# Kernel tuning notes

Measured on AMD Instinct MI355X. Metric: run time of the kernel, lower is better.

## Reference

```python
import jax, jax.numpy as jnp
import numpy as np

N_NODES = 10000
N_EDGES = 160000
MUL = 128            # multiplicity of 0e and 1o node feature irreps
N_RADIAL = 8
AVG_NEIGH = 16.0
INV_SQRT3 = float(1.0 / np.sqrt(3.0))  # w3j(1,1,0) contraction factor (component norm)


def setup_inputs() -> dict:
    key = jax.random.key(0)
    ks = jax.random.split(key, 16)
    node_feats = jax.random.normal(ks[0], (N_NODES, MUL + 3 * MUL), jnp.float32)
    edge_attrs = jax.random.normal(ks[1], (N_EDGES, 4), jnp.float32)      # sph harms l=0,1
    edge_feats = jax.random.normal(ks[2], (N_EDGES, N_RADIAL), jnp.float32)
    lengths = jax.random.uniform(ks[3], (N_EDGES, 1), jnp.float32)
    edge_index = jax.random.randint(ks[4], (2, N_EDGES), 0, N_NODES)
    d_in = 2 * MUL + N_RADIAL + 1  # 265: sender scalars + receiver scalars + radial + length
    def lin(k, sh):
        return jax.random.normal(k, sh, jnp.float32) / np.sqrt(sh[0])
    # last MLP layer: variance_scaling(scale=1e-6, fan_avg, uniform)
    fan_avg = (MUL + 4 * MUL) / 2.0
    lim = float(np.sqrt(3.0 * (0.001 ** 2) / fan_avg))
    return dict(
        node_feats=node_feats, edge_attrs=edge_attrs, edge_feats=edge_feats,
        lengths=lengths, edge_index=edge_index,
        W_scalar=lin(ks[5], (MUL, MUL)),
        W_up0=lin(ks[6], (MUL, MUL)),
        W_up1=lin(ks[7], (MUL, MUL)),
        W_mlp1=lin(ks[8], (d_in, MUL)), b_mlp1=jnp.zeros((MUL,), jnp.float32),
        W_mlp2=lin(ks[9], (MUL, MUL)), b_mlp2=jnp.zeros((MUL,), jnp.float32),
        W_mlp3=jax.random.uniform(ks[10], (MUL, 4 * MUL), jnp.float32, -lim, lim),
        W_out0=lin(ks[11], (2 * MUL, MUL)),
        W_out1=lin(ks[12], (2 * MUL, MUL)),
    )


def reference(node_feats, edge_attrs, edge_feats, lengths, edge_index,
              W_scalar, W_up0, W_up1, W_mlp1, b_mlp1, W_mlp2, b_mlp2, W_mlp3,
              W_out0, W_out1):
    sender, receiver = edge_index[0], edge_index[1]
    s_in = node_feats[:, :MUL]                        # [N, 128] 0e
    v_in = node_feats[:, MUL:].reshape(-1, MUL, 3)    # [N, 128, 3] 1o
    inv = 1.0 / np.sqrt(MUL)
    # linear_scalar / linear_up (e3nn Linear, element path normalization)
    node_scalars = (s_in @ W_scalar) * inv            # [N, 128]
    s_up = (s_in @ W_up0) * inv                       # [N, 128]
    v_up = jnp.einsum('nui,uw->nwi', v_in, W_up1) * inv  # [N, 128, 3]
    # per-edge MLP -> tensor-product weights (Dense-SiLU-Dense-SiLU-Dense)
    mlp_in = jnp.concatenate([node_scalars[sender], node_scalars[receiver],
                              edge_feats, lengths], axis=-1)  # [E, 265]
    h = jax.nn.silu(mlp_in @ W_mlp1 + b_mlp1)
    h = jax.nn.silu(h @ W_mlp2 + b_mlp2)
    tpw = h @ W_mlp3                                  # [E, 512]
    w0, w1, w2, w3 = jnp.split(tpw, 4, axis=-1)       # one [E,128] block per TP path
    # gather sender features; split edge sph harms
    se = s_up[sender]                                 # [E, 128]
    ve = v_up[sender]                                 # [E, 128, 3]
    y0 = edge_attrs[:, 0:1]                           # [E, 1]
    y1 = edge_attrs[:, 1:4]                           # [E, 3]
    # equivariant 'uvu' tensor product (component irrep normalization)
    m0a = w0 * se * y0                                                # 0e x 0e -> 0e
    m0b = w3 * jnp.einsum('eui,ei->eu', ve, y1) * INV_SQRT3           # 1o x 1o -> 0e
    m1a = (w1 * se)[:, :, None] * y1[:, None, :]                      # 0e x 1o -> 1o
    m1b = (w2 * y0)[:, :, None] * ve                                  # 1o x 0e -> 1o
    mji = jnp.concatenate([m0a, m0b,
                           m1a.reshape(N_EDGES, -1),
                           m1b.reshape(N_EDGES, -1)], axis=-1)        # [E, 1024]
    # scatter-sum aggregate over receivers
    msg = jax.ops.segment_sum(mji, receiver, num_segments=N_NODES)    # [N, 1024]
    ms = msg[:, :2 * MUL]                             # [N, 256]  (two 0e blocks)
    mv = msg[:, 2 * MUL:].reshape(-1, 2 * MUL, 3)     # [N, 256, 3] (two 1o blocks)
    # final e3nn Linear (irreps_mid -> target) then / avg_num_neighbors
    inv2 = 1.0 / np.sqrt(2 * MUL)
    out_s = (ms @ W_out0) * (inv2 / AVG_NEIGH)                        # [N, 128]
    out_v = jnp.einsum('nui,uw->nwi', mv, W_out1) * (inv2 / AVG_NEIGH)  # [N, 128, 3]
    # reshape_irreps: [N, mul, (lmax+1)^2] = [N, 128, 4]
    return jnp.concatenate([out_s[:, :, None], out_v], axis=-1)
```

## Files before the change

### kernel.cpp

```cpp
#include <hip/hip_runtime.h>

#define N_NODESC 10000
#define N_EDGESC 160000
#define NBLK_TOT 2500
#define NP       (N_NODESC*128)
#define INV128   0.08838834764831845f
#define INV_SQRT3C 0.5773502691896258f
#define SCALE_OUT 0.00390625f

typedef __attribute__((ext_vector_type(8))) short bf16x8;
typedef __attribute__((ext_vector_type(4))) float f32x4;

__device__ __forceinline__ float silu_f(float x) {
  return x / (1.f + __expf(-x));
}
__device__ __forceinline__ ushort f2bf_rne(float x) {
  uint u = __float_as_uint(x);
  uint r = (u + 0x7FFFu + ((u >> 16) & 1u)) >> 16;
  return (ushort)r;
}
__device__ __forceinline__ float bf2f(ushort h) {
  return __uint_as_float(((uint)h) << 16);
}

__global__ __launch_bounds__(256) void k_hist(const int* __restrict__ eidx,
                                              int* __restrict__ deg) {
  int e = blockIdx.x * 256 + threadIdx.x;
  if (e < N_EDGESC) atomicAdd(&deg[eidx[N_EDGESC + e]], 1);
}

__global__ __launch_bounds__(1024) void k_scan(const int* __restrict__ deg,
                                               int* __restrict__ row_start,
                                               int* __restrict__ cursor) {
  __shared__ int buf[1024];
  const int t = threadIdx.x;
  for (int i = t; i < N_NODESC; i += 1024) cursor[i] = 0;
  int d[10];
  int loc = 0;
  #pragma unroll
  for (int i = 0; i < 10; i++) {
    int n = t * 10 + i;
    d[i] = (n < N_NODESC) ? deg[n] : 0;
    loc += d[i];
  }
  buf[t] = loc;
  __syncthreads();
  int v = loc;
  for (int off = 1; off < 1024; off <<= 1) {
    int u = (t >= off) ? buf[t - off] : 0;
    __syncthreads();
    v += u;
    buf[t] = v;
    __syncthreads();
  }
  int run = v - loc;
  #pragma unroll
  for (int i = 0; i < 10; i++) {
    int n = t * 10 + i;
    if (n < N_NODESC) row_start[n] = run;
    run += d[i];
  }
  if (t == 1023) row_start[N_NODESC] = v;
}

__global__ __launch_bounds__(256) void k_scatter(const int* __restrict__ eidx,
                                                 const int* __restrict__ row_start,
                                                 int* __restrict__ cursor,
                                                 int* __restrict__ perm) {
  int e = blockIdx.x * 256 + threadIdx.x;
  if (e < N_EDGESC) {
    int r = eidx[N_EDGESC + e];
    int pos = row_start[r] + atomicAdd(&cursor[r], 1);
    perm[pos] = e;
  }
}

__global__ __launch_bounds__(256) void k_sortseg(int* __restrict__ perm,
                                                 const int* __restrict__ row_start) {
  int n = blockIdx.x * 256 + threadIdx.x;
  if (n >= N_NODESC) return;
  int s = row_start[n], e = row_start[n + 1];
  for (int i = s + 1; i < e; i++) {
    int key = perm[i];
    int j = i - 1;
    while (j >= s && perm[j] > key) { perm[j + 1] = perm[j]; j--; }
    perm[j + 1] = key;
  }
}

__global__ __launch_bounds__(256) void k_wcomp(
    const float* __restrict__ Wsc, const float* __restrict__ W1,
    ushort* __restrict__ TT) {
  __shared__ float sA2[64][132];
  __shared__ float sW2[128][128];
  const int rh = blockIdx.x;
  const int wb = blockIdx.y;
  for (int idx = threadIdx.x; idx < 128 * 32; idx += 256) {
    int k = idx >> 5, fc = (idx & 31) << 2;
    *(float4*)&sW2[k][fc] = *(const float4*)&W1[(wb * 128 + k) * 128 + fc];
  }
  for (int idx = threadIdx.x; idx < 64 * 32; idx += 256) {
    int i = idx >> 5, fc = (idx & 31) << 2;
    *(float4*)&sA2[i][fc] = *(const float4*)&Wsc[(rh * 64 + i) * 128 + fc];
  }
  __syncthreads();
  const int r0 = (threadIdx.x >> 4) * 4;
  const int c0 = (threadIdx.x & 15) * 8;
  float acc[4][8] = {};
  #pragma unroll 4
  for (int k = 0; k < 128; k++) {
    float a[4];
    #pragma unroll
    for (int j = 0; j < 4; j++) a[j] = sA2[r0 + j][k];
    float w[8];
    *(float4*)&w[0] = *(const float4*)&sW2[k][c0];
    *(float4*)&w[4] = *(const float4*)&sW2[k][c0 + 4];
    #pragma unroll
    for (int j = 0; j < 4; j++)
      #pragma unroll
      for (int c = 0; c < 8; c++) acc[j][c] += a[j] * w[c];
  }
  #pragma unroll
  for (int j = 0; j < 4; j++) {
    int u = rh * 64 + r0 + j;
    #pragma unroll
    for (int c = 0; c < 8; c++) {
      float v = acc[j][c];
      ushort hi = f2bf_rne(v);
      TT[(wb * 2 + 0) * 16384 + (c0 + c) * 128 + u] = hi;
      TT[(wb * 2 + 1) * 16384 + (c0 + c) * 128 + u] = f2bf_rne(v - bf2f(hi));
    }
  }
}

__global__ __launch_bounds__(256) void k_wprep(
    const float* __restrict__ W2, const float* __restrict__ W3,
    const float* __restrict__ Wu0, const float* __restrict__ Wu1,
    const float* __restrict__ Wo0, const float* __restrict__ Wo1,
    ushort* __restrict__ TT) {
  int id = blockIdx.x * 256 + threadIdx.x;
  if (id < 16384) {
    int k = id >> 7, n = id & 127;
    float v = W2[k * 128 + n];
    ushort hi = f2bf_rne(v);
    TT[4 * 16384 + n * 128 + k] = hi;
    TT[5 * 16384 + n * 128 + k] = f2bf_rne(v - bf2f(hi));
  } else if (id < 81920) {
    int s = id - 16384;
    int k = s >> 9, col = s & 511;
    int cb = col >> 7, n = col & 127;
    TT[(6 + cb) * 16384 + n * 128 + k] = f2bf_rne(W3[k * 512 + col]);
  } else if (id < 114688) {
    int t = id - 81920;
    int w = t >> 14, r = t & 16383;
    int k = r >> 7, n = r & 127;
    const float* W = w ? Wu1 : Wu0;
    float v = W[k * 128 + n];
    ushort hi = f2bf_rne(v);
    TT[(10 + w * 2) * 16384 + n * 128 + k] = hi;
    TT[(11 + w * 2) * 16384 + n * 128 + k] = f2bf_rne(v - bf2f(hi));
  } else if (id < 180224) {
    int t = id - 114688;
    int w = t >> 15, r = t & 32767;
    int k = r >> 7, n = r & 127;
    const float* W = w ? Wo1 : Wo0;
    float v = W[k * 128 + n];
    int kh = k >> 7, kk = k & 127;
    ushort hi = f2bf_rne(v);
    TT[(16 + w * 4 + kh * 2) * 16384 + n * 128 + kk] = hi;
    TT[(17 + w * 4 + kh * 2) * 16384 + n * 128 + kk] = f2bf_rne(v - bf2f(hi));
  }
}

#define GEMM_PASS1(ACC)                                                        \
  _Pragma("unroll") for (int s = 0; s < 4; s++) {                              \
    bf16x8 ah = *(const bf16x8*)&sAh[ar][s * 32 + lq * 8];                     \
    _Pragma("unroll") for (int nt = 0; nt < 8; nt++) {                         \
      bf16x8 bb = *(const bf16x8*)&sB[nt * 16 + ln][s * 32 + lq * 8];          \
      ACC[nt] = __builtin_amdgcn_mfma_f32_16x16x32_bf16(ah, bb, ACC[nt], 0, 0, 0); \
    }                                                                          \
  }

#define STAGEB(T) { uint4 tv[8];                                               \
  _Pragma("unroll") for (int i = 0; i < 8; i++)                                \
    tv[i] = ttp[(T) * 2048 + cid + 256 * i];                                   \
  _Pragma("unroll") for (int i = 0; i < 8; i++) {                              \
    int c = cid + 256 * i;                                                     \
    *(uint4*)&sB[c >> 4][(c & 15) * 8] = tv[i]; } }

__global__ __launch_bounds__(256, 3) void k_node_up(
    const float* __restrict__ nf,
    const ushort* __restrict__ TT,
    float* __restrict__ P1s,
    float* __restrict__ P1r,
    float* __restrict__ SU,
    float* __restrict__ VU)
{
  __shared__ ushort sAh[64][132];
  __shared__ ushort sB[128][132];
  const int n0 = blockIdx.x * 64;
  const int which = blockIdx.y;
  const int cid = threadIdx.x;
  const int wid = cid >> 6;
  const int lane = cid & 63;
  const int lq = lane >> 4;
  const int ln = lane & 15;
  const int ar = wid * 16 + ln;
  const uint4* ttp = (const uint4*)TT;

  if (which == 0) {
    for (int idx = cid; idx < 64 * 32; idx += 256) {
      int r = idx >> 5, fc = (idx & 31) << 2;
      int n = n0 + r;
      float4 v = {0.f, 0.f, 0.f, 0.f};
      if (n < N_NODESC) v = *(const float4*)&nf[(size_t)n * 512 + fc];
      float vv[4] = {v.x, v.y, v.z, v.w};
      #pragma unroll
      for (int j = 0; j < 4; j++) sAh[r][fc + j] = f2bf_rne(vv[j]);
    }
    for (int g = 0; g < 3; g++) {
      if (g) __syncthreads();
      const int tA = (g == 2) ? 10 : g * 2;
      STAGEB(tA)
      __syncthreads();
      f32x4 acc[8];
      #pragma unroll
      for (int nt = 0; nt < 8; nt++) acc[nt] = (f32x4){0.f, 0.f, 0.f, 0.f};
      GEMM_PASS1(acc)
      __syncthreads();
      STAGEB(tA + 1)
      __syncthreads();
      GEMM_PASS1(acc)
      float* op = (g == 0) ? P1s : ((g == 1) ? P1r : SU);
      #pragma unroll
      for (int q = 0; q < 4; q++) {
        int n = n0 + wid * 16 + lq * 4 + q;
        if (n < N_NODESC) {
          #pragma unroll
          for (int nt = 0; nt < 8; nt++)
            op[(size_t)n * 128 + nt * 16 + ln] = acc[nt][q] * INV128;
        }
      }
    }
  } else {
    int comp = which - 1;
    for (int idx = cid; idx < 64 * 128; idx += 256) {
      int r = idx >> 7, u = idx & 127;
      int n = n0 + r;
      float v = (n < N_NODESC) ? nf[(size_t)n * 512 + 128 + u * 3 + comp] : 0.f;
      sAh[r][u] = f2bf_rne(v);
    }
    STAGEB(12)
    __syncthreads();
    f32x4 acc[8];
    #pragma unroll
    for (int nt = 0; nt < 8; nt++) acc[nt] = (f32x4){0.f, 0.f, 0.f, 0.f};
    GEMM_PASS1(acc)
    __syncthreads();
    STAGEB(13)
    __syncthreads();
    GEMM_PASS1(acc)
    float* op = VU + (size_t)comp * NP;
    #pragma unroll
    for (int q = 0; q < 4; q++) {
      int n = n0 + wid * 16 + lq * 4 + q;
      if (n < N_NODESC) {
        #pragma unroll
        for (int nt = 0; nt < 8; nt++)
          op[(size_t)n * 128 + nt * 16 + ln] = acc[nt][q] * INV128;
      }
    }
  }
}

#define REDUCE(P, MI) {                                                        \
  const int ntask = sNseg << 7;                                                \
  for (int task = cid; task < ntask; task += 256) {                            \
    const int si = task >> 7, col = task & 127;                                \
    const int s = sSegStart[si], e = sSegStart[si + 1];                        \
    float sum = 0.f;                                                           \
    int e2 = s;                                                                \
    for (; e2 + 8 <= e; e2 += 8) {                                             \
      float m0 = sMsg[e2][col],     m1 = sMsg[e2 + 1][col];                    \
      float m2 = sMsg[e2 + 2][col], m3 = sMsg[e2 + 3][col];                    \
      float m4 = sMsg[e2 + 4][col], m5 = sMsg[e2 + 5][col];                    \
      float m6 = sMsg[e2 + 6][col], m7 = sMsg[e2 + 7][col];                    \
      if ((MI) >= 0) {                                                         \
        const int mi = (MI) >= 0 ? (MI) : 0;                                   \
        sum += m0 * sY4[e2][mi];     sum += m1 * sY4[e2 + 1][mi];              \
        sum += m2 * sY4[e2 + 2][mi]; sum += m3 * sY4[e2 + 3][mi];              \
        sum += m4 * sY4[e2 + 4][mi]; sum += m5 * sY4[e2 + 5][mi];              \
        sum += m6 * sY4[e2 + 6][mi]; sum += m7 * sY4[e2 + 7][mi];              \
      } else { sum += m0; sum += m1; sum += m2; sum += m3;                     \
               sum += m4; sum += m5; sum += m6; sum += m7; }                   \
    }                                                                          \
    for (; e2 < e; e2++) {                                                     \
      float mv = sMsg[e2][col];                                                \
      sum += ((MI) >= 0) ? mv * sY4[e2][(MI) >= 0 ? (MI) : 0] : mv;            \
    }                                                                          \
    if (si == 0 && contF)                                                      \
      CONT[(size_t)gblk * 1024 + (P) * 128 + col] = sum;                       \
    else                                                                       \
      MSG[(size_t)(P) * NP + (size_t)sSegNode[si] * 128 + col] = sum;          \
  } }

#define REDUCE3 {                                                              \
  const int ntask = sNseg << 7;                                                \
  for (int task = cid; task < ntask; task += 256) {                            \
    const int si = task >> 7, col = task & 127;                                \
    const int s = sSegStart[si], e = sSegStart[si + 1];                        \
    float s0 = 0.f, s1 = 0.f, s2 = 0.f;                                        \
    int e2 = s;                                                                \
    for (; e2 + 4 <= e; e2 += 4) {                                             \
      _Pragma("unroll") for (int u = 0; u < 4; u++) {                          \
        float mv = sMsg[e2 + u][col];                                          \
        s0 += mv * sY4[e2 + u][1];                                             \
        s1 += mv * sY4[e2 + u][2];                                             \
        s2 += mv * sY4[e2 + u][3];                                             \
      }                                                                        \
    }                                                                          \
    for (; e2 < e; e2++) {                                                     \
      float mv = sMsg[e2][col];                                                \
      s0 += mv * sY4[e2][1]; s1 += mv * sY4[e2][2]; s2 += mv * sY4[e2][3];     \
    }                                                                          \
    if (si == 0 && contF) {                                                    \
      CONT[(size_t)gblk * 1024 + 2 * 128 + col] = s0;                          \
      CONT[(size_t)gblk * 1024 + 3 * 128 + col] = s1;                          \
      CONT[(size_t)gblk * 1024 + 4 * 128 + col] = s2;                          \
    } else {                                                                   \
      size_t nb = (size_t)sSegNode[si] * 128 + col;                            \
      MSG[2 * (size_t)NP + nb] = s0;                                           \
      MSG[3 * (size_t)NP + nb] = s1;                                           \
      MSG[4 * (size_t)NP + nb] = s2;                                           \
    }                                                                          \
  } }

__global__ __launch_bounds__(256, 3) void k_edge_fused(
    const float* __restrict__ P1s,
    const float* __restrict__ P1r,
    const float* __restrict__ SU,
    const float* __restrict__ VU,
    const float* __restrict__ ef,
    const float* __restrict__ len,
    const float* __restrict__ ea,
    const int* __restrict__ eidx,
    const int* __restrict__ perm,
    const int* __restrict__ row_start,
    const float* __restrict__ W1,
    const float* __restrict__ b1,
    const float* __restrict__ b2,
    const ushort* __restrict__ TT,
    float* __restrict__ MSG,
    float* __restrict__ CONT)
{
  __shared__ ushort sAh[64][132];
  __shared__ ushort sB[128][132];
  __shared__ float sY4[64][4];
  __shared__ int sSnd[64], sRcv[64], sEid[64];
  __shared__ int sSegStart[65], sSegNode[64];
  __shared__ int sNseg, sContFirst;
  float (*sMsg)[132] = (float (*)[132])&sB[0][0];

  const int bid = blockIdx.x;
  const int xcd = bid & 7, sub = bid >> 3;
  const int gblk = (xcd < 4) ? (xcd * 313 + sub)
                             : (1252 + (xcd - 4) * 312 + sub);
  const int j0 = gblk * 64;
  const int cid = threadIdx.x;
  const int wid = cid >> 6;
  const int lane = cid & 63;
  const int lq = lane >> 4;
  const int ln = lane & 15;
  const int ar = wid * 16 + ln;
  const uint4* ttp = (const uint4*)TT;

  if (cid < 64) {
    int r = cid;
    int e = perm[j0 + r];
    int snd = eidx[e];
    int rcv = eidx[N_EDGESC + e];
    sSnd[r] = snd;
    sRcv[r] = rcv;
    sEid[r] = e;
    *(float4*)&sY4[r][0] = *(const float4*)&ea[(size_t)e * 4];
    int prev = __shfl_up(rcv, 1);
    bool flag = (r == 0) || (rcv != prev);
    unsigned long long mask = __ballot(flag ? 1 : 0);
    if (flag) {
      int rank = __popcll(mask & ((1ull << r) - 1ull));
      sSegStart[rank] = r;
      sSegNode[rank] = rcv;
    }
    if (r == 0) {
      sNseg = __popcll(mask);
      sContFirst = (row_start[rcv] != j0) ? 1 : 0;
    }
    if (r == 63) sSegStart[__popcll(mask)] = 64;
  }
  __syncthreads();
  const bool contF = (sContFirst != 0);

  for (int idx = cid; idx < 64 * 32; idx += 256) {
    int r = idx >> 5, c4 = (idx & 31) << 2;
    int ns = sSnd[r], nr = sRcv[r];
    float4 a = *(const float4*)&P1s[(size_t)ns * 128 + c4];
    float4 b = *(const float4*)&P1r[(size_t)nr * 128 + c4];
    int e = sEid[r];
    float el[9];
    float4 e0 = *(const float4*)&ef[(size_t)e * 8];
    float4 e1 = *(const float4*)&ef[(size_t)e * 8 + 4];
    el[0] = e0.x; el[1] = e0.y; el[2] = e0.z; el[3] = e0.w;
    el[4] = e1.x; el[5] = e1.y; el[6] = e1.z; el[7] = e1.w;
    el[8] = len[e];
    float4 bb = *(const float4*)&b1[c4];
    float v[4] = {a.x + b.x + bb.x, a.y + b.y + bb.y,
                  a.z + b.z + bb.z, a.w + b.w + bb.w};
    #pragma unroll
    for (int t = 0; t < 9; t++) {
      float4 wt = *(const float4*)&W1[(size_t)(256 + t) * 128 + c4];
      float elt = el[t];
      v[0] += elt * wt.x; v[1] += elt * wt.y;
      v[2] += elt * wt.z; v[3] += elt * wt.w;
    }
    #pragma unroll
    for (int j = 0; j < 4; j++)
      sAh[r][c4 + j] = f2bf_rne(silu_f(v[j]));
  }
  STAGEB(4)
  __syncthreads();

  f32x4 acc2[8];
  #pragma unroll
  for (int nt = 0; nt < 8; nt++) acc2[nt] = (f32x4){0.f, 0.f, 0.f, 0.f};
  GEMM_PASS1(acc2)
  __syncthreads();
  STAGEB(5)
  __syncthreads();
  GEMM_PASS1(acc2)
  __syncthreads();
  #pragma unroll
  for (int nt = 0; nt < 8; nt++) {
    int col = nt * 16 + ln;
    float bb2 = b2[col];
    #pragma unroll
    for (int q = 0; q < 4; q++) {
      int rr = wid * 16 + lq * 4 + q;
      sAh[rr][col] = f2bf_rne(silu_f(acc2[nt][q] + bb2));
    }
  }

  int erow[4], esnd[4];
  float y0r[4], y1r3[4][3];
  #pragma unroll
  for (int q = 0; q < 4; q++) {
    int rr = wid * 16 + lq * 4 + q;
    erow[q] = rr;
    esnd[q] = sSnd[rr];
    y0r[q] = sY4[rr][0];
    #pragma unroll
    for (int i = 0; i < 3; i++) y1r3[q][i] = sY4[rr][1 + i];
  }
  float se[4][8];
  #pragma unroll
  for (int q = 0; q < 4; q++)
    #pragma unroll
    for (int nt = 0; nt < 8; nt++)
      se[q][nt] = SU[(size_t)esnd[q] * 128 + nt * 16 + ln];
  float dacc[4][8];

  STAGEB(6)
  __syncthreads();

  {
    f32x4 acc3[8];
    #pragma unroll
    for (int nt = 0; nt < 8; nt++) acc3[nt] = (f32x4){0.f, 0.f, 0.f, 0.f};
    GEMM_PASS1(acc3)
    __syncthreads();
    #pragma unroll
    for (int q = 0; q < 4; q++)
      #pragma unroll
      for (int nt = 0; nt < 8; nt++)
        sMsg[erow[q]][nt * 16 + ln] = acc3[nt][q] * se[q][nt] * y0r[q];
    __syncthreads();
    REDUCE(0, -1)
    __syncthreads();
    STAGEB(7)
    __syncthreads();
  }
  {
    f32x4 acc3[8];
    #pragma unroll
    for (int nt = 0; nt < 8; nt++) acc3[nt] = (f32x4){0.f, 0.f, 0.f, 0.f};
    GEMM_PASS1(acc3)
    __syncthreads();
    #pragma unroll
    for (int q = 0; q < 4; q++)
      #pragma unroll
      for (int nt = 0; nt < 8; nt++)
        sMsg[erow[q]][nt * 16 + ln] = acc3[nt][q] * se[q][nt];
    __syncthreads();
    REDUCE3
    __syncthreads();
    STAGEB(8)
    __syncthreads();
  }
  {
    f32x4 acc3[8];
    #pragma unroll
    for (int nt = 0; nt < 8; nt++) acc3[nt] = (f32x4){0.f, 0.f, 0.f, 0.f};
    GEMM_PASS1(acc3)
    __syncthreads();
    for (int pi = 0; pi < 3; pi++) {
      float vu[4][8];
      #pragma unroll
      for (int q = 0; q < 4; q++)
        #pragma unroll
        for (int nt = 0; nt < 8; nt++) {
          vu[q][nt] = VU[(size_t)pi * NP + (size_t)esnd[q] * 128 + nt * 16 + ln];
          if (pi == 0) dacc[q][nt] = vu[q][nt] * y1r3[q][0];
          else dacc[q][nt] += vu[q][nt] * y1r3[q][pi];
        }
      #pragma unroll
      for (int q = 0; q < 4; q++)
        #pragma unroll
        for (int nt = 0; nt < 8; nt++)
          sMsg[erow[q]][nt * 16 + ln] = acc3[nt][q] * vu[q][nt];
      __syncthreads();
      if (pi == 0) { REDUCE(5, 0) }
      else if (pi == 1) { REDUCE(6, 0) }
      else { REDUCE(7, 0) }
      __syncthreads();
    }
    STAGEB(9)
    __syncthreads();
  }
  {
    f32x4 acc3[8];
    #pragma unroll
    for (int nt = 0; nt < 8; nt++) acc3[nt] = (f32x4){0.f, 0.f, 0.f, 0.f};
    GEMM_PASS1(acc3)
    __syncthreads();
    #pragma unroll
    for (int q = 0; q < 4; q++)
      #pragma unroll
      for (int nt = 0; nt < 8; nt++)
        sMsg[erow[q]][nt * 16 + ln] = acc3[nt][q] * dacc[q][nt] * INV_SQRT3C;
    __syncthreads();
    REDUCE(1, -1)
  }
}

__global__ __launch_bounds__(256) void k_fixup(float* __restrict__ MSG,
                                               const float* __restrict__ CONT,
                                               const int* __restrict__ row_start) {
  int t = blockIdx.x * 256 + threadIdx.x;
  int n = t >> 5;
  int c4 = (t & 31) * 4;
  if (n >= N_NODESC) return;
  int s = row_start[n], e = row_start[n + 1];
  if (e <= s) return;
  int b0 = s >> 6, b1 = (e - 1) >> 6;
  if (b1 <= b0) return;
  for (int p = 0; p < 8; p++) {
    float4 v = *(float4*)&MSG[(size_t)p * NP + (size_t)n * 128 + c4];
    for (int b = b0 + 1; b <= b1; b++) {
      const float4 u = *(const float4*)&CONT[(size_t)b * 1024 + p * 128 + c4];
      v.x += u.x; v.y += u.y; v.z += u.z; v.w += u.w;
    }
    *(float4*)&MSG[(size_t)p * NP + (size_t)n * 128 + c4] = v;
  }
}

__global__ __launch_bounds__(256, 3) void k_out(
    const float* __restrict__ MSG,
    const ushort* __restrict__ TT,
    float* __restrict__ out)
{
  __shared__ ushort sAh[64][132];
  __shared__ ushort sB[128][132];
  const int n0 = blockIdx.x * 64;
  const int y = blockIdx.y;
  const int cid = threadIdx.x;
  const int wid = cid >> 6;
  const int lane = cid & 63;
  const int lq = lane >> 4;
  const int ln = lane & 15;
  const int ar = wid * 16 + ln;
  const uint4* ttp = (const uint4*)TT;
  const int pA = (y == 0) ? 0 : (1 + y);
  const int pB = (y == 0) ? 1 : (4 + y);
  const int tbase = 16 + ((y == 0) ? 0 : 4);

  f32x4 acc[8];
  #pragma unroll
  for (int nt = 0; nt < 8; nt++) acc[nt] = (f32x4){0.f, 0.f, 0.f, 0.f};

  for (int kh = 0; kh < 2; kh++) {
    if (kh) __syncthreads();
    const int p = kh ? pB : pA;
    for (int idx = cid; idx < 64 * 32; idx += 256) {
      int r = idx >> 5, fc = (idx & 31) << 2;
      int n = n0 + r;
      float4 v = {0.f, 0.f, 0.f, 0.f};
      if (n < N_NODESC) v = *(const float4*)&MSG[(size_t)p * NP + (size_t)n * 128 + fc];
      float vv[4] = {v.x, v.y, v.z, v.w};
      #pragma unroll
      for (int j = 0; j < 4; j++) sAh[r][fc + j] = f2bf_rne(vv[j]);
    }
    STAGEB(tbase + kh * 2)
    __syncthreads();
    GEMM_PASS1(acc)
    __syncthreads();
    STAGEB(tbase + kh * 2 + 1)
    __syncthreads();
    GEMM_PASS1(acc)
  }
  #pragma unroll
  for (int q = 0; q < 4; q++) {
    int n = n0 + wid * 16 + lq * 4 + q;
    if (n < N_NODESC) {
      #pragma unroll
      for (int nt = 0; nt < 8; nt++)
        out[(size_t)n * 512 + (size_t)(nt * 16 + ln) * 4 + y] = acc[nt][q] * SCALE_OUT;
    }
  }
}

extern "C" void kernel_launch(void* const* d_in, const int* in_sizes, int n_in,
                              void* d_out, int out_size, void* d_ws, size_t ws_size,
                              hipStream_t stream) {
  const float* nf  = (const float*)d_in[0];
  const float* ea  = (const float*)d_in[1];
  const float* ef  = (const float*)d_in[2];
  const float* len = (const float*)d_in[3];
  const int*   ei  = (const int*)d_in[4];
  const float* Wsc = (const float*)d_in[5];
  const float* Wu0 = (const float*)d_in[6];
  const float* Wu1 = (const float*)d_in[7];
  const float* W1  = (const float*)d_in[8];
  const float* b1  = (const float*)d_in[9];
  const float* W2  = (const float*)d_in[10];
  const float* b2  = (const float*)d_in[11];
  const float* W3  = (const float*)d_in[12];
  const float* Wo0 = (const float*)d_in[13];
  const float* Wo1 = (const float*)d_in[14];
  float* out = (float*)d_out;
  float* ws  = (float*)d_ws;

  const size_t NPs = (size_t)NP;
  float* P1s  = ws;
  float* P1r  = ws + NPs;
  float* SU   = ws + 2 * NPs;
  float* VU   = ws + 3 * NPs;
  float* MSG  = ws + 6 * NPs;
  float* CONT = ws + 14 * NPs;
  ushort* TT  = (ushort*)(CONT + (size_t)NBLK_TOT * 1024);
  int* perm      = (int*)(TT + 24 * 16384);
  int* deg       = perm + N_EDGESC;
  int* cursor    = deg + N_NODESC;
  int* row_start = cursor + N_NODESC;

  hipMemsetAsync(deg, 0, N_NODESC * sizeof(int), stream);
  hipMemsetAsync(MSG, 0, 8 * NPs * sizeof(float), stream);

  k_hist<<<(N_EDGESC + 255) / 256, 256, 0, stream>>>(ei, deg);
  k_scan<<<1, 1024, 0, stream>>>(deg, row_start, cursor);
  k_scatter<<<(N_EDGESC + 255) / 256, 256, 0, stream>>>(ei, row_start, cursor, perm);
  k_sortseg<<<(N_NODESC + 255) / 256, 256, 0, stream>>>(perm, row_start);
  k_wcomp<<<dim3(2, 2), 256, 0, stream>>>(Wsc, W1, TT);
  k_wprep<<<704, 256, 0, stream>>>(W2, W3, Wu0, Wu1, Wo0, Wo1, TT);

  k_node_up<<<dim3(157, 4), 256, 0, stream>>>(nf, TT, P1s, P1r, SU, VU);

  k_edge_fused<<<NBLK_TOT, 256, 0, stream>>>(P1s, P1r, SU, VU, ef, len, ea, ei,
                                             perm, row_start, W1, b1, b2, TT,
                                             MSG, CONT);

  k_fixup<<<(N_NODESC * 32 + 255) / 256, 256, 0, stream>>>(MSG, CONT, row_start);
  k_out<<<dim3(157, 4), 256, 0, stream>>>(MSG, TT, out);
}
```

Measured before the change: 312.6 us.

## Merge small preprocessing kernels and drop the message-buffer memset

Folds the degree histogram into the weight-prep kernel, and the per-segment insertion sort into k_node_up as an extra grid slice, which cuts two kernel launches. The 8*NP-float memset of MSG is removed; k_fixup now writes zeros for nodes with no incoming edges. This relies on k_edge_fused writing every MSG row that has edges, and the sort running inside node_up is correct only because that kernel does not read perm.

```diff
diff --git a/kernel.cpp b/kernel.cpp
--- a/kernel.cpp
+++ b/kernel.cpp
@@ -23,122 +23,19 @@
   return __uint_as_float(((uint)h) << 16);
 }
 
-__global__ __launch_bounds__(256) void k_hist(const int* __restrict__ eidx,
-                                              int* __restrict__ deg) {
-  int e = blockIdx.x * 256 + threadIdx.x;
-  if (e < N_EDGESC) atomicAdd(&deg[eidx[N_EDGESC + e]], 1);
-}
-
-__global__ __launch_bounds__(1024) void k_scan(const int* __restrict__ deg,
-                                               int* __restrict__ row_start,
-                                               int* __restrict__ cursor) {
-  __shared__ int buf[1024];
-  const int t = threadIdx.x;
-  for (int i = t; i < N_NODESC; i += 1024) cursor[i] = 0;
-  int d[10];
-  int loc = 0;
-  #pragma unroll
-  for (int i = 0; i < 10; i++) {
-    int n = t * 10 + i;
-    d[i] = (n < N_NODESC) ? deg[n] : 0;
-    loc += d[i];
-  }
-  buf[t] = loc;
-  __syncthreads();
-  int v = loc;
-  for (int off = 1; off < 1024; off <<= 1) {
-    int u = (t >= off) ? buf[t - off] : 0;
-    __syncthreads();
-    v += u;
-    buf[t] = v;
-    __syncthreads();
-  }
-  int run = v - loc;
-  #pragma unroll
-  for (int i = 0; i < 10; i++) {
-    int n = t * 10 + i;
-    if (n < N_NODESC) row_start[n] = run;
-    run += d[i];
-  }
-  if (t == 1023) row_start[N_NODESC] = v;
-}
-
-__global__ __launch_bounds__(256) void k_scatter(const int* __restrict__ eidx,
-                                                 const int* __restrict__ row_start,
-                                                 int* __restrict__ cursor,
-                                                 int* __restrict__ perm) {
-  int e = blockIdx.x * 256 + threadIdx.x;
-  if (e < N_EDGESC) {
-    int r = eidx[N_EDGESC + e];
-    int pos = row_start[r] + atomicAdd(&cursor[r], 1);
-    perm[pos] = e;
-  }
-}
-
-__global__ __launch_bounds__(256) void k_sortseg(int* __restrict__ perm,
-                                                 const int* __restrict__ row_start) {
-  int n = blockIdx.x * 256 + threadIdx.x;
-  if (n >= N_NODESC) return;
-  int s = row_start[n], e = row_start[n + 1];
-  for (int i = s + 1; i < e; i++) {
-    int key = perm[i];
-    int j = i - 1;
-    while (j >= s && perm[j] > key) { perm[j + 1] = perm[j]; j--; }
-    perm[j + 1] = key;
-  }
-}
-
-__global__ __launch_bounds__(256) void k_wcomp(
-    const float* __restrict__ Wsc, const float* __restrict__ W1,
-    ushort* __restrict__ TT) {
-  __shared__ float sA2[64][132];
-  __shared__ float sW2[128][128];
-  const int rh = blockIdx.x;
-  const int wb = blockIdx.y;
-  for (int idx = threadIdx.x; idx < 128 * 32; idx += 256) {
-    int k = idx >> 5, fc = (idx & 31) << 2;
-    *(float4*)&sW2[k][fc] = *(const float4*)&W1[(wb * 128 + k) * 128 + fc];
-  }
-  for (int idx = threadIdx.x; idx < 64 * 32; idx += 256) {
-    int i = idx >> 5, fc = (idx & 31) << 2;
-    *(float4*)&sA2[i][fc] = *(const float4*)&Wsc[(rh * 64 + i) * 128 + fc];
-  }
-  __syncthreads();
-  const int r0 = (threadIdx.x >> 4) * 4;
-  const int c0 = (threadIdx.x & 15) * 8;
-  float acc[4][8] = {};
-  #pragma unroll 4
-  for (int k = 0; k < 128; k++) {
-    float a[4];
-    #pragma unroll
-    for (int j = 0; j < 4; j++) a[j] = sA2[r0 + j][k];
-    float w[8];
-    *(float4*)&w[0] = *(const float4*)&sW2[k][c0];
-    *(float4*)&w[4] = *(const float4*)&sW2[k][c0 + 4];
-    #pragma unroll
-    for (int j = 0; j < 4; j++)
-      #pragma unroll
-      for (int c = 0; c < 8; c++) acc[j][c] += a[j] * w[c];
-  }
-  #pragma unroll
-  for (int j = 0; j < 4; j++) {
-    int u = rh * 64 + r0 + j;
-    #pragma unroll
-    for (int c = 0; c < 8; c++) {
-      float v = acc[j][c];
-      ushort hi = f2bf_rne(v);
-      TT[(wb * 2 + 0) * 16384 + (c0 + c) * 128 + u] = hi;
-      TT[(wb * 2 + 1) * 16384 + (c0 + c) * 128 + u] = f2bf_rne(v - bf2f(hi));
-    }
-  }
-}
-
-__global__ __launch_bounds__(256) void k_wprep(
+__global__ __launch_bounds__(256) void k_histprep(
+    const int* __restrict__ eidx, int* __restrict__ deg,
     const float* __restrict__ W2, const float* __restrict__ W3,
     const float* __restrict__ Wu0, const float* __restrict__ Wu1,
     const float* __restrict__ Wo0, const float* __restrict__ Wo1,
     ushort* __restrict__ TT) {
-  int id = blockIdx.x * 256 + threadIdx.x;
+  const int bid = blockIdx.x;
+  if (bid < 625) {
+    int e = bid * 256 + threadIdx.x;
+    if (e < N_EDGESC) atomicAdd(&deg[eidx[N_EDGESC + e]], 1);
+    return;
+  }
+  int id = (bid - 625) * 256 + threadIdx.x;
   if (id < 16384) {
     int k = id >> 7, n = id & 127;
     float v = W2[k * 128 + n];
@@ -172,6 +69,97 @@
   }
 }
 
+__global__ __launch_bounds__(1024) void k_scan(const int* __restrict__ deg,
+                                               int* __restrict__ row_start,
+                                               int* __restrict__ cursor) {
+  __shared__ int buf[1024];
+  const int t = threadIdx.x;
+  for (int i = t; i < N_NODESC; i += 1024) cursor[i] = 0;
+  int d[10];
+  int loc = 0;
+  #pragma unroll
+  for (int i = 0; i < 10; i++) {
+    int n = t * 10 + i;
+    d[i] = (n < N_NODESC) ? deg[n] : 0;
+    loc += d[i];
+  }
+  buf[t] = loc;
+  __syncthreads();
+  int v = loc;
+  for (int off = 1; off < 1024; off <<= 1) {
+    int u = (t >= off) ? buf[t - off] : 0;
+    __syncthreads();
+    v += u;
+    buf[t] = v;
+    __syncthreads();
+  }
+  int run = v - loc;
+  #pragma unroll
+  for (int i = 0; i < 10; i++) {
+    int n = t * 10 + i;
+    if (n < N_NODESC) row_start[n] = run;
+    run += d[i];
+  }
+  if (t == 1023) row_start[N_NODESC] = v;
+}
+
+__global__ __launch_bounds__(256) void k_scatter(const int* __restrict__ eidx,
+                                                 const int* __restrict__ row_start,
+                                                 int* __restrict__ cursor,
+                                                 int* __restrict__ perm) {
+  int e = blockIdx.x * 256 + threadIdx.x;
+  if (e < N_EDGESC) {
+    int r = eidx[N_EDGESC + e];
+    int pos = row_start[r] + atomicAdd(&cursor[r], 1);
+    perm[pos] = e;
+  }
+}
+
+__global__ __launch_bounds__(256) void k_wcomp(
+    const float* __restrict__ Wsc, const float* __restrict__ W1,
+    ushort* __restrict__ TT) {
+  __shared__ float sA2[64][132];
+  __shared__ float sW2[128][128];
+  const int rh = blockIdx.x;
+  const int wb = blockIdx.y;
+  for (int idx = threadIdx.x; idx < 128 * 32; idx += 256) {
+    int k = idx >> 5, fc = (idx & 31) << 2;
+    *(float4*)&sW2[k][fc] = *(const float4*)&W1[(wb * 128 + k) * 128 + fc];
+  }
+  for (int idx = threadIdx.x; idx < 64 * 32; idx += 256) {
+    int i = idx >> 5, fc = (idx & 31) << 2;
+    *(float4*)&sA2[i][fc] = *(const float4*)&Wsc[(rh * 64 + i) * 128 + fc];
+  }
+  __syncthreads();
+  const int r0 = (threadIdx.x >> 4) * 4;
+  const int c0 = (threadIdx.x & 15) * 8;
+  float acc[4][8] = {};
+  #pragma unroll 4
+  for (int k = 0; k < 128; k++) {
+    float a[4];
+    #pragma unroll
+    for (int j = 0; j < 4; j++) a[j] = sA2[r0 + j][k];
+    float w[8];
+    *(float4*)&w[0] = *(const float4*)&sW2[k][c0];
+    *(float4*)&w[4] = *(const float4*)&sW2[k][c0 + 4];
+    #pragma unroll
+    for (int j = 0; j < 4; j++)
+      #pragma unroll
+      for (int c = 0; c < 8; c++) acc[j][c] += a[j] * w[c];
+  }
+  #pragma unroll
+  for (int j = 0; j < 4; j++) {
+    int u = rh * 64 + r0 + j;
+    #pragma unroll
+    for (int c = 0; c < 8; c++) {
+      float v = acc[j][c];
+      ushort hi = f2bf_rne(v);
+      TT[(wb * 2 + 0) * 16384 + (c0 + c) * 128 + u] = hi;
+      TT[(wb * 2 + 1) * 16384 + (c0 + c) * 128 + u] = f2bf_rne(v - bf2f(hi));
+    }
+  }
+}
+
 #define GEMM_PASS1(ACC)                                                        \
   _Pragma("unroll") for (int s = 0; s < 4; s++) {                              \
     bf16x8 ah = *(const bf16x8*)&sAh[ar][s * 32 + lq * 8];                     \
@@ -194,7 +182,9 @@
     float* __restrict__ P1s,
     float* __restrict__ P1r,
     float* __restrict__ SU,
-    float* __restrict__ VU)
+    float* __restrict__ VU,
+    int* __restrict__ perm,
+    const int* __restrict__ row_start)
 {
   __shared__ ushort sAh[64][132];
   __shared__ ushort sB[128][132];
@@ -207,6 +197,20 @@
   const int ln = lane & 15;
   const int ar = wid * 16 + ln;
   const uint4* ttp = (const uint4*)TT;
+
+  if (which == 4) {
+    int n = blockIdx.x * 256 + cid;
+    if (n < N_NODESC) {
+      int s = row_start[n], e = row_start[n + 1];
+      for (int i = s + 1; i < e; i++) {
+        int key = perm[i];
+        int j = i - 1;
+        while (j >= s && perm[j] > key) { perm[j + 1] = perm[j]; j--; }
+        perm[j + 1] = key;
+      }
+    }
+    return;
+  }
 
   if (which == 0) {
     for (int idx = cid; idx < 64 * 32; idx += 256) {
@@ -559,7 +563,13 @@
   int c4 = (t & 31) * 4;
   if (n >= N_NODESC) return;
   int s = row_start[n], e = row_start[n + 1];
-  if (e <= s) return;
+  if (e <= s) {
+    float4 z = {0.f, 0.f, 0.f, 0.f};
+    #pragma unroll
+    for (int p = 0; p < 8; p++)
+      *(float4*)&MSG[(size_t)p * NP + (size_t)n * 128 + c4] = z;
+    return;
+  }
   int b0 = s >> 6, b1 = (e - 1) >> 6;
   if (b1 <= b0) return;
   for (int p = 0; p < 8; p++) {
@@ -662,16 +672,14 @@
   int* row_start = cursor + N_NODESC;
 
   hipMemsetAsync(deg, 0, N_NODESC * sizeof(int), stream);
-  hipMemsetAsync(MSG, 0, 8 * NPs * sizeof(float), stream);
-
-  k_hist<<<(N_EDGESC + 255) / 256, 256, 0, stream>>>(ei, deg);
+
+  k_histprep<<<1329, 256, 0, stream>>>(ei, deg, W2, W3, Wu0, Wu1, Wo0, Wo1, TT);
   k_scan<<<1, 1024, 0, stream>>>(deg, row_start, cursor);
   k_scatter<<<(N_EDGESC + 255) / 256, 256, 0, stream>>>(ei, row_start, cursor, perm);
-  k_sortseg<<<(N_NODESC + 255) / 256, 256, 0, stream>>>(perm, row_start);
   k_wcomp<<<dim3(2, 2), 256, 0, stream>>>(Wsc, W1, TT);
-  k_wprep<<<704, 256, 0, stream>>>(W2, W3, Wu0, Wu1, Wo0, Wo1, TT);
-
-  k_node_up<<<dim3(157, 4), 256, 0, stream>>>(nf, TT, P1s, P1r, SU, VU);
+
+  k_node_up<<<dim3(157, 5), 256, 0, stream>>>(nf, TT, P1s, P1r, SU, VU,
+                                              perm, row_start);
 
   k_edge_fused<<<NBLK_TOT, 256, 0, stream>>>(P1s, P1r, SU, VU, ef, len, ea, ei,
                                              perm, row_start, W1, b1, b2, TT,
```

Measured after the change: 285.2 us (median of 2 runs). 8.8% less time.
